# Performance work log

Measured on AMD Instinct MI355X. Metric: run time of the kernel, lower is better.

Reference implementation:

```python
import jax, jax.numpy as jnp
import numpy as np

# LIF constants from norse.LIFParameters in the module
DT = 1e-3
TAU_MEM_INV = 4.0      # 1 / tau_mem, tau_mem = 0.25
TAU_SYN_INV = 200.0    # norse default 1/5e-3
V_TH = 0.1
ALPHA = 50.0           # super-spike surrogate slope
NHEAD = 4

@jax.custom_vjp
def spike(x):
    # SuperSpike: heaviside forward, surrogate gradient backward
    return (x > 0).astype(x.dtype)

def _spike_fwd(x):
    return spike(x), x

def _spike_bwd(x, g):
    return (g / (ALPHA * jnp.abs(x) + 1.0) ** 2,)

spike.defvjp(_spike_fwd, _spike_bwd)

def lif_reservoir(x, Win, Wres):
    # x: [B,S,I] -> spikes z: [B,S,R]. All batches start from zero state,
    # so the per-batch python loop of the original vectorizes over B.
    inp = jnp.einsum('bsi,ir->bsr', x, Win)  # precompute input currents
    B, S, R = inp.shape

    def step(carry, cur):  # cur: [B,R]
        v, i, z = carry
        total = cur + z @ Wres  # z=0 at t=0, matching the t>0 branch
        v_dec = v + DT * TAU_MEM_INV * (-v + i)  # v_leak = 0
        i_dec = i * (1.0 - DT * TAU_SYN_INV)
        z_new = spike(v_dec - V_TH)
        v_new = (1.0 - z_new) * v_dec            # v_reset = 0
        i_new = i_dec + total
        return (v_new, i_new, z_new), z_new

    init = (jnp.zeros((B, R), x.dtype),) * 3
    _, zs = jax.lax.scan(step, init, jnp.swapaxes(inp, 0, 1))
    return jnp.swapaxes(zs, 0, 1)  # [B,S,R]

def layer_norm(x, g, b, eps=1e-5):
    m = x.mean(-1, keepdims=True)
    v = ((x - m) ** 2).mean(-1, keepdims=True)
    return (x - m) / jnp.sqrt(v + eps) * g + b

def encoder_layer(x, Wqkv, bqkv, Wo, bo, g1, b1, g2, b2, W1, c1, W2, c2):
    # Post-norm TransformerEncoderLayer, relu activation, dropout=eval(0)
    B, S, D = x.shape
    dh = D // NHEAD
    qkv = x @ Wqkv.T + bqkv
    q, k, v = jnp.split(qkv, 3, axis=-1)
    rh = lambda t: t.reshape(B, S, NHEAD, dh)
    q, k, v = rh(q), rh(k), rh(v)
    scores = jnp.einsum('bqhd,bkhd->bhqk', q, k) / jnp.sqrt(jnp.asarray(dh, x.dtype))
    attn = jax.nn.softmax(scores, axis=-1)
    o = jnp.einsum('bhqk,bkhd->bqhd', attn, v).reshape(B, S, D)
    o = o @ Wo.T + bo
    x = layer_norm(x + o, g1, b1)
    ff = jax.nn.relu(x @ W1.T + c1) @ W2.T + c2
    return layer_norm(x + ff, g2, b2)

def setup_inputs() -> dict:
    key = jax.random.key(0)
    B, S, I, R, D, L, FF = 32, 1024, 8, 512, 256, 2, 1024
    ks = jax.random.split(key, 16)
    x = jax.random.normal(ks[0], (B, S, I), jnp.float32)
    Win = jax.random.normal(ks[1], (I, R), jnp.float32) * 0.1
    # sparse reservoir: density 0.2, values uniform [0,1)
    mask = (jax.random.uniform(ks[2], (R, R)) < 0.2).astype(jnp.float32)
    Wres = jax.random.uniform(ks[3], (R, R), jnp.float32) * mask
    Wread = jax.random.normal(ks[4], (D, R), jnp.float32) * 0.04
    bread = jnp.zeros((D,), jnp.float32)
    Wqkv = jax.random.normal(ks[5], (L, 3 * D, D), jnp.float32) * 0.05
    bqkv = jnp.zeros((L, 3 * D), jnp.float32)
    Wo = jax.random.normal(ks[6], (L, D, D), jnp.float32) * 0.05
    bo = jnp.zeros((L, D), jnp.float32)
    ln1_g = jnp.ones((L, D), jnp.float32)
    ln1_b = jnp.zeros((L, D), jnp.float32)
    ln2_g = jnp.ones((L, D), jnp.float32)
    ln2_b = jnp.zeros((L, D), jnp.float32)
    Wff1 = jax.random.normal(ks[7], (L, FF, D), jnp.float32) * 0.05
    bff1 = jnp.zeros((L, FF), jnp.float32)
    Wff2 = jax.random.normal(ks[8], (L, D, FF), jnp.float32) * 0.05
    bff2 = jnp.zeros((L, D), jnp.float32)
    return dict(x=x, Win=Win, Wres=Wres, Wread=Wread, bread=bread,
                Wqkv=Wqkv, bqkv=bqkv, Wo=Wo, bo=bo,
                ln1_g=ln1_g, ln1_b=ln1_b, ln2_g=ln2_g, ln2_b=ln2_b,
                Wff1=Wff1, bff1=bff1, Wff2=Wff2, bff2=bff2)

def reference(x, Win, Wres, Wread, bread, Wqkv, bqkv, Wo, bo,
              ln1_g, ln1_b, ln2_g, ln2_b, Wff1, bff1, Wff2, bff2):
    z = lif_reservoir(x, Win, Wres)          # [B,S,R] spike trains
    h = z @ Wread.T + bread                  # readout to transformer_dim
    for l in range(Wqkv.shape[0]):           # fixed small num_layers
        h = encoder_layer(h, Wqkv[l], bqkv[l], Wo[l], bo[l],
                          ln1_g[l], ln1_b[l], ln2_g[l], ln2_b[l],
                          Wff1[l], bff1[l], Wff2[l], bff2[l])
    return h
```

## Files before the change

### kernel.cpp

```cpp
#include <hip/hip_runtime.h>
#include <stdint.h>

using short8  = __attribute__((ext_vector_type(8))) short;
using floatx4 = __attribute__((ext_vector_type(4))) float;

typedef unsigned short u16;
typedef unsigned int u32;
typedef unsigned long long u64;

#define AS1(p) ((const __attribute__((address_space(1))) void*)(p))
#define AS3(p) ((__attribute__((address_space(3))) void*)(p))

__device__ __forceinline__ float bs2f(u16 u) { return __uint_as_float(((u32)u) << 16); }
__device__ __forceinline__ u16 f2bs(float f) {
  u32 x = __float_as_uint(f);
  x += 0x7FFFu + ((x >> 16) & 1u);
  return (u16)(x >> 16);
}
__device__ __forceinline__ float lo16(u32 u) { return __uint_as_float(u << 16); }
__device__ __forceinline__ float hi16(u32 u) { return __uint_as_float(u & 0xFFFF0000u); }

__global__ __launch_bounds__(256) void cvt_k(const float* __restrict__ src,
                                             u16* __restrict__ dst, int n) {
  int i = blockIdx.x * 256 + threadIdx.x;
  if (i < n) dst[i] = f2bs(src[i]);
}

__global__ __launch_bounds__(512) void inp_k(const float* __restrict__ x,
                                             const float* __restrict__ Win,
                                             float* __restrict__ inp) {
  const int row = blockIdx.x;
  const int r = threadIdx.x;
  const float* xr = x + (size_t)row * 8;
  float s = 0.f;
#pragma unroll
  for (int k = 0; k < 8; ++k) s = fmaf(Win[k * 512 + r], xr[k], s);
  inp[(size_t)row * 512 + r] = s;
}

__global__ __launch_bounds__(64) void reservoir_k(
    const float* __restrict__ inp,
    const float* __restrict__ Wres,
    u16* __restrict__ zout)
{
  const int b = blockIdx.x;
  const int c = threadIdx.x & 63;
  const float* ib = inp + (size_t)b * 524288 + c * 8;
  u16* zb = zout + (size_t)b * 524288 + c * 8;
  float v[8] = {}, ci[8] = {}, rec[8] = {};
  u32 pz = 0;
  float4 pa[8], pc[8];
#pragma unroll
  for (int u = 0; u < 8; ++u) {
    pa[u] = *(const float4*)(ib + (size_t)u * 512);
    pc[u] = *(const float4*)(ib + (size_t)u * 512 + 4);
  }
  for (int tb = 0; tb < 128; ++tb) {
    float4 na[8], nc[8];
    if (tb < 127) {
      const float* nb = ib + (size_t)(tb + 1) * 4096;
#pragma unroll
      for (int u = 0; u < 8; ++u) {
        na[u] = *(const float4*)(nb + (size_t)u * 512);
        nc[u] = *(const float4*)(nb + (size_t)u * 512 + 4);
      }
    }
#pragma unroll
    for (int u = 0; u < 8; ++u) {
      const int t = tb * 8 + u;
      const float in[8] = {pa[u].x, pa[u].y, pa[u].z, pa[u].w,
                           pc[u].x, pc[u].y, pc[u].z, pc[u].w};
      u32 nzb = 0;
      u32 zw[4];
#pragma unroll
      for (int j = 0; j < 8; ++j) {
        const float vdec = __fadd_rn(v[j], __fmul_rn(0.004f, __fadd_rn(-v[j], ci[j])));
        const int zc = (__fadd_rn(vdec, -0.1f) > 0.f) ? 1 : 0;
        v[j] = zc ? 0.f : vdec;
        nzb |= (u32)zc << j;
        ci[j] = __fadd_rn(__fmul_rn(ci[j], 0.8f), __fadd_rn(in[j], rec[j]));
        if (j & 1) zw[j >> 1] |= zc ? 0x3F800000u : 0u;
        else       zw[j >> 1]  = zc ? 0x3F80u : 0u;
      }
      *(uint4*)(zb + (size_t)t * 512) = make_uint4(zw[0], zw[1], zw[2], zw[3]);
      const u64 anyt = __ballot((nzb ^ pz) != 0);
      if (anyt) {
#pragma unroll
        for (int j = 0; j < 8; ++j) {
          const u64 nm = __ballot((nzb >> j) & 1);
          const u64 pm = __ballot((pz >> j) & 1);
          u64 on   = nm & ~pm;
          u64 offm = pm & ~nm;
          while (on) {
            const int cc = __builtin_ctzll(on); on &= on - 1;
            const float* wr = Wres + ((size_t)(cc * 8 + j) << 9) + c * 8;
            const float4 w0 = *(const float4*)wr;
            const float4 w1 = *(const float4*)(wr + 4);
            rec[0] += w0.x; rec[1] += w0.y; rec[2] += w0.z; rec[3] += w0.w;
            rec[4] += w1.x; rec[5] += w1.y; rec[6] += w1.z; rec[7] += w1.w;
          }
          while (offm) {
            const int cc = __builtin_ctzll(offm); offm &= offm - 1;
            const float* wr = Wres + ((size_t)(cc * 8 + j) << 9) + c * 8;
            const float4 w0 = *(const float4*)wr;
            const float4 w1 = *(const float4*)(wr + 4);
            rec[0] -= w0.x; rec[1] -= w0.y; rec[2] -= w0.z; rec[3] -= w0.w;
            rec[4] -= w1.x; rec[5] -= w1.y; rec[6] -= w1.z; rec[7] -= w1.w;
          }
        }
      }
      pz = nzb;
    }
    if (tb < 127) {
#pragma unroll
      for (int u = 0; u < 8; ++u) { pa[u] = na[u]; pc[u] = nc[u]; }
    }
  }
}

enum { MODE_BF16 = 0, MODE_F32 = 1, MODE_DUAL = 2, MODE_QKV = 3 };

template <int WM, int WN, int MODE>
__global__ __launch_bounds__(WM * WN * 64) void gemm_bt(
    const u16* __restrict__ A, const u16* __restrict__ B,
    const float* __restrict__ bias, void* __restrict__ C0,
    void* __restrict__ C1, void* __restrict__ C2, int K, int lda, int ldb,
    int ldc, long long sA, long long sB, long long sC, float scale, int relu)
{
  constexpr int BM = WM * 64, BN = WN * 64, BK = 32;
  constexpr int NT = WM * WN * 64;
  constexpr int CA = BM * 4 / NT, CB = BN * 4 / NT;
  __shared__ __align__(16) u16 As[BM * BK];
  __shared__ __align__(16) u16 Bs[BN * BK];
  const int tid = threadIdx.x;
  const int bz = blockIdx.z;
  const u16* Ab = A + (size_t)bz * sA + (size_t)blockIdx.y * BM * lda;
  const u16* Bb = B + (size_t)bz * sB + (size_t)blockIdx.x * BN * ldb;
  const int wavei = tid >> 6, lane = tid & 63;
  const int r16 = lane & 15, quad = lane >> 4;
  const int wm = (wavei % WM) * 64, wn = (wavei / WM) * 64;
  floatx4 acc[4][4] = {};
  for (int k0 = 0; k0 < K; k0 += BK) {
#pragma unroll
    for (int c = 0; c < CA; ++c) {
      const int idx = c * NT + tid;
      const int row = idx >> 2, kc = (idx & 3) << 3;
      __builtin_amdgcn_global_load_lds(AS1(Ab + (size_t)row * lda + k0 + kc),
                                       AS3(As + idx * 8), 16, 0, 0);
    }
#pragma unroll
    for (int c = 0; c < CB; ++c) {
      const int idx = c * NT + tid;
      const int row = idx >> 2, kc = (idx & 3) << 3;
      __builtin_amdgcn_global_load_lds(AS1(Bb + (size_t)row * ldb + k0 + kc),
                                       AS3(Bs + idx * 8), 16, 0, 0);
    }
    __syncthreads();
    short8 af[4], bfr[4];
#pragma unroll
    for (int i = 0; i < 4; ++i)
      af[i] = *(const short8*)&As[(wm + i * 16 + r16) * BK + quad * 8];
#pragma unroll
    for (int i = 0; i < 4; ++i)
      bfr[i] = *(const short8*)&Bs[(wn + i * 16 + r16) * BK + quad * 8];
#pragma unroll
    for (int i = 0; i < 4; ++i)
#pragma unroll
      for (int j = 0; j < 4; ++j)
        acc[i][j] = __builtin_amdgcn_mfma_f32_16x16x32_bf16(af[i], bfr[j], acc[i][j], 0, 0, 0);
    __syncthreads();
  }
#pragma unroll
  for (int i = 0; i < 4; ++i) {
#pragma unroll
    for (int j = 0; j < 4; ++j) {
#pragma unroll
      for (int q = 0; q < 4; ++q) {
        const int m = blockIdx.y * BM + wm + i * 16 + quad * 4 + q;
        const int n = blockIdx.x * BN + wn + j * 16 + r16;
        float val = acc[i][j][q] * scale;
        if (bias) val += bias[n];
        if (relu) val = fmaxf(val, 0.f);
        if constexpr (MODE == MODE_BF16) {
          ((u16*)C0)[(size_t)bz * sC + (size_t)m * ldc + n] = f2bs(val);
        } else if constexpr (MODE == MODE_F32) {
          ((float*)C0)[(size_t)m * ldc + n] = val;
        } else if constexpr (MODE == MODE_DUAL) {
          ((float*)C0)[(size_t)m * ldc + n] = val;
          ((u16*)C1)[(size_t)m * ldc + n] = f2bs(val);
        } else if constexpr (MODE == MODE_QKV) {
          const int b = m >> 10, s = m & 1023;
          const u16 outv = f2bs(val);
          const int h = (n & 255) >> 6, d = n & 63;
          if (n < 256)
            ((u16*)C0)[(((size_t)(b * 4 + h)) * 1024 + s) * 64 + d] = outv;
          else if (n < 512)
            ((u16*)C1)[(((size_t)(b * 4 + h)) * 1024 + s) * 64 + d] = outv;
          else
            ((u16*)C2)[(((size_t)(b * 4 + h)) * 64 + d) * 1024 + s] = outv;
        }
      }
    }
  }
}

__global__ __launch_bounds__(256) void attn_k(
    const u16* __restrict__ q_s,
    const u16* __restrict__ k_s,
    const u16* __restrict__ v_t,
    u16* __restrict__ o16)
{
  constexpr int LQ = 72, LV = 136, LP = 136;
  __shared__ __align__(16) u16 Qs[128 * LQ];
  __shared__ __align__(16) u16 Ks[128 * LQ];
  __shared__ __align__(16) u16 Vt[64 * LV];
  __shared__ __align__(16) u16 Ps[128 * LP];
  const int tid = threadIdx.x;
  const int w = tid >> 6, lane = tid & 63;
  const int r16 = lane & 15, quad = lane >> 4;
  const int p = blockIdx.y;
  const int q0 = blockIdx.x * 128;
  const u16* qg = q_s + ((size_t)p * 1024 + q0) * 64;
  const u16* kg = k_s + (size_t)p * 65536;
  const u16* vg = v_t + (size_t)p * 65536;

#pragma unroll
  for (int it = 0; it < 4; ++it) {
    const int idx = it * 256 + tid;
    const int row = idx >> 3, c8 = (idx & 7) * 8;
    *(uint4*)&Qs[row * LQ + c8] = *(const uint4*)(qg + (size_t)row * 64 + c8);
    *(uint4*)&Ks[row * LQ + c8] = *(const uint4*)(kg + (size_t)row * 64 + c8);
  }
#pragma unroll
  for (int it = 0; it < 4; ++it) {
    const int idx = it * 256 + tid;
    const int row = idx >> 4, c8 = (idx & 15) * 8;
    *(uint4*)&Vt[row * LV + c8] = *(const uint4*)(vg + (size_t)row * 1024 + c8);
  }
  __syncthreads();

  short8 aq[2][2];
#pragma unroll
  for (int i = 0; i < 2; ++i)
#pragma unroll
    for (int kc = 0; kc < 2; ++kc)
      aq[i][kc] = *(const short8*)&Qs[(w * 32 + i * 16 + r16) * LQ + kc * 32 + quad * 8];

  floatx4 o[2][4] = {};
  float mr[2][4], l[2][4];
#pragma unroll
  for (int i = 0; i < 2; ++i)
#pragma unroll
    for (int q = 0; q < 4; ++q) { mr[i][q] = -3e38f; l[i][q] = 0.f; }

  for (int kt = 0; kt < 8; ++kt) {
    uint4 kpre[4], vpre[4];
    if (kt < 7) {
      const u16* kgn = kg + (size_t)(kt + 1) * 128 * 64;
#pragma unroll
      for (int it = 0; it < 4; ++it) {
        const int idx = it * 256 + tid;
        kpre[it] = *(const uint4*)(kgn + (size_t)(idx >> 3) * 64 + (idx & 7) * 8);
        vpre[it] = *(const uint4*)(vg + (size_t)(idx >> 4) * 1024 + (kt + 1) * 128 + (idx & 15) * 8);
      }
    }
    floatx4 s[2][8] = {};
#pragma unroll
    for (int kc = 0; kc < 2; ++kc) {
#pragma unroll
      for (int f = 0; f < 8; ++f) {
        const short8 bk = *(const short8*)&Ks[(f * 16 + r16) * LQ + kc * 32 + quad * 8];
#pragma unroll
        for (int i = 0; i < 2; ++i)
          s[i][f] = __builtin_amdgcn_mfma_f32_16x16x32_bf16(aq[i][kc], bk, s[i][f], 0, 0, 0);
      }
    }
#pragma unroll
    for (int i = 0; i < 2; ++i) {
      float mt[4] = {-3e38f, -3e38f, -3e38f, -3e38f};
#pragma unroll
      for (int f = 0; f < 8; ++f)
#pragma unroll
        for (int q = 0; q < 4; ++q) {
          s[i][f][q] *= 0.125f;
          mt[q] = fmaxf(mt[q], s[i][f][q]);
        }
#pragma unroll
      for (int off = 8; off > 0; off >>= 1)
#pragma unroll
        for (int q = 0; q < 4; ++q) mt[q] = fmaxf(mt[q], __shfl_xor(mt[q], off));
      float al[4], rs[4] = {};
#pragma unroll
      for (int q = 0; q < 4; ++q) {
        const float mn = fmaxf(mr[i][q], mt[q]);
        al[q] = __expf(mr[i][q] - mn);
        mr[i][q] = mn;
      }
#pragma unroll
      for (int f = 0; f < 8; ++f)
#pragma unroll
        for (int q = 0; q < 4; ++q) {
          const float pv = __expf(s[i][f][q] - mr[i][q]);
          s[i][f][q] = pv;
          rs[q] += pv;
        }
#pragma unroll
      for (int off = 8; off > 0; off >>= 1)
#pragma unroll
        for (int q = 0; q < 4; ++q) rs[q] += __shfl_xor(rs[q], off);
#pragma unroll
      for (int q = 0; q < 4; ++q) l[i][q] = l[i][q] * al[q] + rs[q];
#pragma unroll
      for (int n = 0; n < 4; ++n)
#pragma unroll
        for (int q = 0; q < 4; ++q) o[i][n][q] *= al[q];
#pragma unroll
      for (int f = 0; f < 8; ++f)
#pragma unroll
        for (int q = 0; q < 4; ++q)
          Ps[(w * 32 + i * 16 + quad * 4 + q) * LP + f * 16 + r16] = f2bs(s[i][f][q]);
    }
#pragma unroll
    for (int kc = 0; kc < 4; ++kc) {
      short8 ap[2];
#pragma unroll
      for (int i = 0; i < 2; ++i)
        ap[i] = *(const short8*)&Ps[(w * 32 + i * 16 + r16) * LP + kc * 32 + quad * 8];
#pragma unroll
      for (int n = 0; n < 4; ++n) {
        const short8 bv = *(const short8*)&Vt[(n * 16 + r16) * LV + kc * 32 + quad * 8];
#pragma unroll
        for (int i = 0; i < 2; ++i)
          o[i][n] = __builtin_amdgcn_mfma_f32_16x16x32_bf16(ap[i], bv, o[i][n], 0, 0, 0);
      }
    }
    __syncthreads();
    if (kt < 7) {
#pragma unroll
      for (int it = 0; it < 4; ++it) {
        const int idx = it * 256 + tid;
        *(uint4*)&Ks[(idx >> 3) * LQ + (idx & 7) * 8] = kpre[it];
        *(uint4*)&Vt[(idx >> 4) * LV + (idx & 15) * 8] = vpre[it];
      }
      __syncthreads();
    }
  }
  const int bb = p >> 2, hh = p & 3;
#pragma unroll
  for (int i = 0; i < 2; ++i)
#pragma unroll
    for (int q = 0; q < 4; ++q) {
      const float inv = 1.f / l[i][q];
      const int srow = q0 + w * 32 + i * 16 + quad * 4 + q;
#pragma unroll
      for (int n = 0; n < 4; ++n)
        o16[((size_t)bb * 1024 + srow) * 256 + hh * 64 + n * 16 + r16] =
            f2bs(o[i][n][q] * inv);
    }
}

__global__ __launch_bounds__(256) void ln_k(const float* __restrict__ x,
                                            const float* __restrict__ add,
                                            const float* __restrict__ g,
                                            const float* __restrict__ bta,
                                            float* __restrict__ y32,
                                            u16* __restrict__ y16) {
  const int row = blockIdx.x * 4 + (threadIdx.x >> 6);
  const int lane = threadIdx.x & 63;
  const size_t base = (size_t)row * 256 + lane * 4;
  const float4 xv = *(const float4*)(x + base);
  const float4 av = *(const float4*)(add + base);
  float sv[4] = {xv.x + av.x, xv.y + av.y, xv.z + av.z, xv.w + av.w};
  float sum = sv[0] + sv[1] + sv[2] + sv[3];
#pragma unroll
  for (int off = 32; off > 0; off >>= 1) sum += __shfl_xor(sum, off);
  const float mean = sum * (1.f / 256.f);
  float var = 0.f;
  float d[4];
#pragma unroll
  for (int i = 0; i < 4; ++i) { d[i] = sv[i] - mean; var += d[i] * d[i]; }
#pragma unroll
  for (int off = 32; off > 0; off >>= 1) var += __shfl_xor(var, off);
  var *= (1.f / 256.f);
  const float inv = 1.f / sqrtf(var + 1e-5f);
  float yv[4];
#pragma unroll
  for (int i = 0; i < 4; ++i)
    yv[i] = d[i] * inv * g[lane * 4 + i] + bta[lane * 4 + i];
  if (y32) *(float4*)(y32 + base) = make_float4(yv[0], yv[1], yv[2], yv[3]);
  if (y16) {
    const u32 p0 = (u32)f2bs(yv[0]) | ((u32)f2bs(yv[1]) << 16);
    const u32 p1 = (u32)f2bs(yv[2]) | ((u32)f2bs(yv[3]) << 16);
    *(uint2*)(y16 + base) = make_uint2(p0, p1);
  }
}

extern "C" void kernel_launch(void* const* d_in, const int* in_sizes, int n_in,
                              void* d_out, int out_size, void* d_ws,
                              size_t ws_size, hipStream_t stream) {
  (void)in_sizes; (void)n_in; (void)out_size; (void)ws_size;
  const float* x     = (const float*)d_in[0];
  const float* Win   = (const float*)d_in[1];
  const float* Wres  = (const float*)d_in[2];
  const float* Wread = (const float*)d_in[3];
  const float* bread = (const float*)d_in[4];
  const float* Wqkv  = (const float*)d_in[5];
  const float* bqkv  = (const float*)d_in[6];
  const float* Wo    = (const float*)d_in[7];
  const float* bo    = (const float*)d_in[8];
  const float* g1    = (const float*)d_in[9];
  const float* b1    = (const float*)d_in[10];
  const float* g2    = (const float*)d_in[11];
  const float* b2    = (const float*)d_in[12];
  const float* W1    = (const float*)d_in[13];
  const float* c1    = (const float*)d_in[14];
  const float* W2    = (const float*)d_in[15];
  const float* c2    = (const float*)d_in[16];

  char* ws = (char*)d_ws;
  size_t off = 0;
  auto carve = [&](size_t bytes) {
    char* p = ws + off;
    off += (bytes + 255) & ~(size_t)255;
    return p;
  };
  u16* z      = (u16*)carve((size_t)32 * 1024 * 512 * 2);
  u16* wrd16  = (u16*)carve((size_t)256 * 512 * 2);
  u16* wqkv16 = (u16*)carve((size_t)2 * 768 * 256 * 2);
  u16* wo16   = (u16*)carve((size_t)2 * 256 * 256 * 2);
  u16* w116   = (u16*)carve((size_t)2 * 1024 * 256 * 2);
  u16* w216   = (u16*)carve((size_t)2 * 256 * 1024 * 2);
  u16* q_s    = (u16*)carve((size_t)128 * 1024 * 64 * 2);
  u16* k_s    = (u16*)carve((size_t)128 * 1024 * 64 * 2);
  u16* v_t    = (u16*)carve((size_t)128 * 64 * 1024 * 2);
  float* h32  = (float*)carve((size_t)32768 * 256 * 4);
  float* lin  = (float*)carve((size_t)32768 * 256 * 4);
  u16* h16    = (u16*)carve((size_t)32768 * 256 * 2);
  u16* ff1    = (u16*)carve((size_t)32768 * 1024 * 2);
  u16* o16    = h16;
  float* inp  = (float*)ff1;

  cvt_k<<<dim3(512), dim3(256), 0, stream>>>(Wread, wrd16, 131072);
  cvt_k<<<dim3(1536), dim3(256), 0, stream>>>(Wqkv, wqkv16, 393216);
  cvt_k<<<dim3(512), dim3(256), 0, stream>>>(Wo, wo16, 131072);
  cvt_k<<<dim3(2048), dim3(256), 0, stream>>>(W1, w116, 524288);
  cvt_k<<<dim3(2048), dim3(256), 0, stream>>>(W2, w216, 524288);

  inp_k<<<dim3(32768), dim3(512), 0, stream>>>(x, Win, inp);
  reservoir_k<<<dim3(32), dim3(64), 0, stream>>>(inp, Wres, z);

  gemm_bt<2, 2, MODE_DUAL><<<dim3(2, 256, 1), dim3(256), 0, stream>>>(
      z, wrd16, bread, h32, h16, nullptr, 512, 512, 512, 256, 0, 0, 0, 1.0f, 0);

  for (int l = 0; l < 2; ++l) {
    gemm_bt<2, 2, MODE_QKV><<<dim3(6, 256, 1), dim3(256), 0, stream>>>(
        h16, wqkv16 + (size_t)l * 196608, bqkv + l * 768, q_s, k_s, v_t, 256,
        256, 256, 0, 0, 0, 0, 1.0f, 0);
    attn_k<<<dim3(8, 128), dim3(256), 0, stream>>>(q_s, k_s, v_t, o16);
    gemm_bt<2, 2, MODE_F32><<<dim3(2, 256, 1), dim3(256), 0, stream>>>(
        o16, wo16 + (size_t)l * 65536, bo + l * 256, lin, nullptr, nullptr,
        256, 256, 256, 256, 0, 0, 0, 1.0f, 0);
    ln_k<<<dim3(8192), dim3(256), 0, stream>>>(h32, lin, g1 + l * 256,
                                               b1 + l * 256, h32, h16);
    gemm_bt<2, 2, MODE_BF16><<<dim3(8, 256, 1), dim3(256), 0, stream>>>(
        h16, w116 + (size_t)l * 262144, c1 + l * 1024, ff1, nullptr, nullptr,
        256, 256, 256, 1024, 0, 0, 0, 1.0f, 1);
    gemm_bt<2, 2, MODE_F32><<<dim3(2, 256, 1), dim3(256), 0, stream>>>(
        ff1, w216 + (size_t)l * 262144, c2 + l * 256, lin, nullptr, nullptr,
        1024, 1024, 1024, 256, 0, 0, 0, 1.0f, 0);
    float* y32 = (l == 1) ? (float*)d_out : h32;
    u16* y16 = (l == 1) ? nullptr : h16;
    ln_k<<<dim3(8192), dim3(256), 0, stream>>>(h32, lin, g2 + l * 256,
                                               b2 + l * 256, y32, y16);
  }
}
```

Before: 1.332 ms.

## Speculate reservoir 8-step blocks without recurrence, replay on spike toggles; fuse weight casts

The reservoir kernel now runs each 8-timestep block on a fast path with no per-step ballots or recurrent-weight updates. It only checks once at the end of the block whether any spike toggled. If one did, it restores the saved state and replays the block with the exact per-step sparse Wres update path. The input prefetch into registers is replaced by in-block loads. The five weight-conversion launches are merged into one kernel to cut launch overhead. The risk is extra recompute when toggles are common and a loss of latency hiding from dropping the double-buffered prefetch.

```diff
diff --git a/kernel.cpp b/kernel.cpp
--- a/kernel.cpp
+++ b/kernel.cpp
@@ -20,10 +20,17 @@
 __device__ __forceinline__ float lo16(u32 u) { return __uint_as_float(u << 16); }
 __device__ __forceinline__ float hi16(u32 u) { return __uint_as_float(u & 0xFFFF0000u); }
 
-__global__ __launch_bounds__(256) void cvt_k(const float* __restrict__ src,
-                                             u16* __restrict__ dst, int n) {
-  int i = blockIdx.x * 256 + threadIdx.x;
-  if (i < n) dst[i] = f2bs(src[i]);
+__global__ __launch_bounds__(256) void cvt_all_k(
+    const float* __restrict__ s0, const float* __restrict__ s1,
+    const float* __restrict__ s2, const float* __restrict__ s3,
+    const float* __restrict__ s4, u16* __restrict__ d0, u16* __restrict__ d1,
+    u16* __restrict__ d2, u16* __restrict__ d3, u16* __restrict__ d4) {
+  const int i = blockIdx.x * 256 + threadIdx.x;
+  if (i < 131072)        d0[i] = f2bs(s0[i]);
+  else if (i < 524288)   d1[i - 131072] = f2bs(s1[i - 131072]);
+  else if (i < 655360)   d2[i - 524288] = f2bs(s2[i - 524288]);
+  else if (i < 1179648)  d3[i - 655360] = f2bs(s3[i - 655360]);
+  else                   d4[i - 1179648] = f2bs(s4[i - 1179648]);
 }
 
 __global__ __launch_bounds__(512) void inp_k(const float* __restrict__ x,
@@ -38,7 +45,7 @@
   inp[(size_t)row * 512 + r] = s;
 }
 
-__global__ __launch_bounds__(64) void reservoir_k(
+__global__ __launch_bounds__(64, 1) void reservoir_k(
     const float* __restrict__ inp,
     const float* __restrict__ Wres,
     u16* __restrict__ zout)
@@ -49,27 +56,25 @@
   u16* zb = zout + (size_t)b * 524288 + c * 8;
   float v[8] = {}, ci[8] = {}, rec[8] = {};
   u32 pz = 0;
-  float4 pa[8], pc[8];
-#pragma unroll
-  for (int u = 0; u < 8; ++u) {
-    pa[u] = *(const float4*)(ib + (size_t)u * 512);
-    pc[u] = *(const float4*)(ib + (size_t)u * 512 + 4);
-  }
   for (int tb = 0; tb < 128; ++tb) {
-    float4 na[8], nc[8];
-    if (tb < 127) {
-      const float* nb = ib + (size_t)(tb + 1) * 4096;
-#pragma unroll
-      for (int u = 0; u < 8; ++u) {
-        na[u] = *(const float4*)(nb + (size_t)u * 512);
-        nc[u] = *(const float4*)(nb + (size_t)u * 512 + 4);
-      }
-    }
+    float4 xa[8], xc[8];
+#pragma unroll
+    for (int u = 0; u < 8; ++u) {
+      const float* p = ib + (size_t)(tb * 8 + u) * 512;
+      xa[u] = *(const float4*)p;
+      xc[u] = *(const float4*)(p + 4);
+    }
+    asm volatile("" ::: "memory");
+    float sv[8], sci[8];
+#pragma unroll
+    for (int j = 0; j < 8; ++j) { sv[j] = v[j]; sci[j] = ci[j]; }
+    const u32 spz = pz;
+    u32 togg = 0;
 #pragma unroll
     for (int u = 0; u < 8; ++u) {
       const int t = tb * 8 + u;
-      const float in[8] = {pa[u].x, pa[u].y, pa[u].z, pa[u].w,
-                           pc[u].x, pc[u].y, pc[u].z, pc[u].w};
+      const float in[8] = {xa[u].x, xa[u].y, xa[u].z, xa[u].w,
+                           xc[u].x, xc[u].y, xc[u].z, xc[u].w};
       u32 nzb = 0;
       u32 zw[4];
 #pragma unroll
@@ -83,37 +88,60 @@
         else       zw[j >> 1]  = zc ? 0x3F80u : 0u;
       }
       *(uint4*)(zb + (size_t)t * 512) = make_uint4(zw[0], zw[1], zw[2], zw[3]);
-      const u64 anyt = __ballot((nzb ^ pz) != 0);
-      if (anyt) {
+      togg |= nzb ^ pz;
+      pz = nzb;
+    }
+    const u64 anyt = __ballot(togg != 0);
+    if (anyt) {
+#pragma unroll
+      for (int j = 0; j < 8; ++j) { v[j] = sv[j]; ci[j] = sci[j]; }
+      pz = spz;
+#pragma unroll 1
+      for (int u = 0; u < 8; ++u) {
+        const int t = tb * 8 + u;
+        const float in[8] = {xa[u].x, xa[u].y, xa[u].z, xa[u].w,
+                             xc[u].x, xc[u].y, xc[u].z, xc[u].w};
+        u32 nzb = 0;
+        u32 zw[4];
 #pragma unroll
         for (int j = 0; j < 8; ++j) {
-          const u64 nm = __ballot((nzb >> j) & 1);
-          const u64 pm = __ballot((pz >> j) & 1);
-          u64 on   = nm & ~pm;
-          u64 offm = pm & ~nm;
-          while (on) {
-            const int cc = __builtin_ctzll(on); on &= on - 1;
-            const float* wr = Wres + ((size_t)(cc * 8 + j) << 9) + c * 8;
-            const float4 w0 = *(const float4*)wr;
-            const float4 w1 = *(const float4*)(wr + 4);
-            rec[0] += w0.x; rec[1] += w0.y; rec[2] += w0.z; rec[3] += w0.w;
-            rec[4] += w1.x; rec[5] += w1.y; rec[6] += w1.z; rec[7] += w1.w;
-          }
-          while (offm) {
-            const int cc = __builtin_ctzll(offm); offm &= offm - 1;
-            const float* wr = Wres + ((size_t)(cc * 8 + j) << 9) + c * 8;
-            const float4 w0 = *(const float4*)wr;
-            const float4 w1 = *(const float4*)(wr + 4);
-            rec[0] -= w0.x; rec[1] -= w0.y; rec[2] -= w0.z; rec[3] -= w0.w;
-            rec[4] -= w1.x; rec[5] -= w1.y; rec[6] -= w1.z; rec[7] -= w1.w;
+          const float vdec = __fadd_rn(v[j], __fmul_rn(0.004f, __fadd_rn(-v[j], ci[j])));
+          const int zc = (__fadd_rn(vdec, -0.1f) > 0.f) ? 1 : 0;
+          v[j] = zc ? 0.f : vdec;
+          nzb |= (u32)zc << j;
+          ci[j] = __fadd_rn(__fmul_rn(ci[j], 0.8f), __fadd_rn(in[j], rec[j]));
+          if (j & 1) zw[j >> 1] |= zc ? 0x3F800000u : 0u;
+          else       zw[j >> 1]  = zc ? 0x3F80u : 0u;
+        }
+        *(uint4*)(zb + (size_t)t * 512) = make_uint4(zw[0], zw[1], zw[2], zw[3]);
+        const u64 a2 = __ballot((nzb ^ pz) != 0);
+        if (a2) {
+#pragma unroll
+          for (int j = 0; j < 8; ++j) {
+            const u64 nm = __ballot((nzb >> j) & 1);
+            const u64 pm = __ballot((pz >> j) & 1);
+            u64 on   = nm & ~pm;
+            u64 offm = pm & ~nm;
+            while (on) {
+              const int cc = __builtin_ctzll(on); on &= on - 1;
+              const float* wr = Wres + ((size_t)(cc * 8 + j) << 9) + c * 8;
+              const float4 w0 = *(const float4*)wr;
+              const float4 w1 = *(const float4*)(wr + 4);
+              rec[0] += w0.x; rec[1] += w0.y; rec[2] += w0.z; rec[3] += w0.w;
+              rec[4] += w1.x; rec[5] += w1.y; rec[6] += w1.z; rec[7] += w1.w;
+            }
+            while (offm) {
+              const int cc = __builtin_ctzll(offm); offm &= offm - 1;
+              const float* wr = Wres + ((size_t)(cc * 8 + j) << 9) + c * 8;
+              const float4 w0 = *(const float4*)wr;
+              const float4 w1 = *(const float4*)(wr + 4);
+              rec[0] -= w0.x; rec[1] -= w0.y; rec[2] -= w0.z; rec[3] -= w0.w;
+              rec[4] -= w1.x; rec[5] -= w1.y; rec[6] -= w1.z; rec[7] -= w1.w;
+            }
           }
         }
-      }
-      pz = nzb;
-    }
-    if (tb < 127) {
-#pragma unroll
-      for (int u = 0; u < 8; ++u) { pa[u] = na[u]; pc[u] = nc[u]; }
+        pz = nzb;
+      }
     }
   }
 }
@@ -440,12 +468,9 @@
   u16* o16    = h16;
   float* inp  = (float*)ff1;
 
-  cvt_k<<<dim3(512), dim3(256), 0, stream>>>(Wread, wrd16, 131072);
-  cvt_k<<<dim3(1536), dim3(256), 0, stream>>>(Wqkv, wqkv16, 393216);
-  cvt_k<<<dim3(512), dim3(256), 0, stream>>>(Wo, wo16, 131072);
-  cvt_k<<<dim3(2048), dim3(256), 0, stream>>>(W1, w116, 524288);
-  cvt_k<<<dim3(2048), dim3(256), 0, stream>>>(W2, w216, 524288);
-
+  cvt_all_k<<<dim3(6656), dim3(256), 0, stream>>>(Wread, Wqkv, Wo, W1, W2,
+                                                  wrd16, wqkv16, wo16, w116,
+                                                  w216);
   inp_k<<<dim3(32768), dim3(512), 0, stream>>>(x, Win, inp);
   reservoir_k<<<dim3(32), dim3(64), 0, stream>>>(inp, Wres, z);
 
```

Result: slower. 1.460 ms (+9.6%).
